# Optimization experiments

Hardware: AMD Instinct MI355X
Metric: run time of the kernel (lower is better)

The kernel has to match this reference:

```python
import jax, jax.numpy as jnp
import numpy as np

S, I, C_M, C_P, C_Z = 128, 384, 256, 32, 128

def setup_inputs() -> dict:
    key = jax.random.key(0)
    ks = jax.random.split(key, 7)
    sc = 1.0 / np.sqrt(C_M)
    return {
        "msa_rep": jax.random.normal(ks[0], (S, I, C_M), jnp.float32),
        "ln_gamma": jnp.ones((C_M,), jnp.float32),
        "ln_beta": jnp.zeros((C_M,), jnp.float32),
        "Wa": jax.random.normal(ks[1], (C_P, C_M), jnp.float32) * sc,
        "Wb": jax.random.normal(ks[2], (C_P, C_M), jnp.float32) * sc,
        "Wproj": jax.random.normal(ks[3], (C_Z, C_P * C_P), jnp.float32) / np.sqrt(C_P * C_P),
        "bproj": jnp.zeros((C_Z,), jnp.float32),
    }

def reference(msa_rep, ln_gamma, ln_beta, Wa, Wb, Wproj, bproj):
    # LayerNorm over last dim (eps matches torch default 1e-5)
    mu = jnp.mean(msa_rep, axis=-1, keepdims=True)
    var = jnp.mean(jnp.square(msa_rep - mu), axis=-1, keepdims=True)
    x = (msa_rep - mu) * jax.lax.rsqrt(var + 1e-5) * ln_gamma + ln_beta
    # Two linear projections (torch Linear: y = x @ W.T), no bias
    a = jnp.einsum('sic,pc->sip', x, Wa)  # [s, i, c_p]
    b = jnp.einsum('sic,pc->sip', x, Wb)  # [s, i, c_p]
    norm = 1.0 / msa_rep.shape[-3]
    # Outer product mean over sequences s -> [i, j, c, d]
    outer = norm * jnp.einsum('sic,sjd->ijcd', a, b)
    outer = outer.reshape(outer.shape[0], outer.shape[1], -1)  # [i, j, c*c]
    return jnp.einsum('ijk,zk->ijz', outer, Wproj) + bproj  # [i, j, c_z]
```

## Files before the change

### kernel.cpp

```cpp
#include <hip/hip_runtime.h>
#include <hip/hip_bf16.h>

typedef short s8v  __attribute__((ext_vector_type(8)));
typedef float f32x4 __attribute__((ext_vector_type(4)));

__device__ __forceinline__ unsigned short f2bf(float f) {
  unsigned int b = __float_as_uint(f);
  b += 0x7fffu + ((b >> 16) & 1u);
  return (unsigned short)(b >> 16);
}

__global__ __launch_bounds__(256) void prep_w_kernel(
    const float* __restrict__ Wa, const float* __restrict__ Wb,
    const float* __restrict__ Wproj,
    unsigned short* __restrict__ wab, unsigned short* __restrict__ wfrag) {
  int gid = blockIdx.x * 256 + threadIdx.x;
  if (gid < 16384) {
    int e = gid;
    int j = e & 7, lane = (e >> 3) & 63, kt = (e >> 9) & 7, nt = e >> 12;
    int p = nt * 16 + (lane & 15);
    int c = kt * 32 + ((lane >> 4) << 3) + j;
    float v = (p < 32) ? Wa[p * 256 + c] : Wb[(p - 32) * 256 + c];
    wab[e] = f2bf(v);
  } else {
    int e = gid - 16384;
    int j = e & 7, lane = (e >> 3) & 63, kt = (e >> 9) & 31, nt = e >> 14;
    int z = nt * 16 + (lane & 15);
    int kp = kt * 32 + ((lane >> 4) << 3) + j;
    int c = kp & 31, d = kp >> 5;
    wfrag[e] = f2bf(Wproj[z * 1024 + c * 32 + d]);
  }
}

#define XS 264
#define OS 66
__global__ __launch_bounds__(256) void kernel_a(
    const float* __restrict__ msa, const float* __restrict__ gamma, const float* __restrict__ beta,
    const unsigned short* __restrict__ wab,
    unsigned short* __restrict__ afrag, unsigned short* __restrict__ bfrag) {
  __shared__ unsigned short xs[64 * XS];
  __shared__ float os[64 * OS];
  const int i  = blockIdx.x >> 1;
  const int sh = blockIdx.x & 1;
  const int tid = threadIdx.x;
  const int w = tid >> 6, lane = tid & 63;
  const int gq = lane >> 4, nlo = lane & 15;

  const float4 g4  = *(const float4*)(gamma + lane * 4);
  const float4 be4 = *(const float4*)(beta  + lane * 4);

  for (int it = 0; it < 16; ++it) {
    const int sl = it * 4 + w;
    const int s  = sh * 64 + sl;
    const float4 v = *(const float4*)(msa + (size_t)(s * 384 + i) * 256 + lane * 4);
    float sum = v.x + v.y + v.z + v.w;
    float sq  = fmaf(v.x, v.x, fmaf(v.y, v.y, fmaf(v.z, v.z, v.w * v.w)));
#pragma unroll
    for (int off = 32; off >= 1; off >>= 1) {
      sum += __shfl_xor(sum, off);
      sq  += __shfl_xor(sq,  off);
    }
    const float mu   = sum * (1.f / 256.f);
    const float var  = sq * (1.f / 256.f) - mu * mu;
    const float rstd = rsqrtf(var + 1e-5f);
    unsigned int lo = (unsigned int)f2bf((v.x - mu) * rstd * g4.x + be4.x)
                    | ((unsigned int)f2bf((v.y - mu) * rstd * g4.y + be4.y) << 16);
    unsigned int hi = (unsigned int)f2bf((v.z - mu) * rstd * g4.z + be4.z)
                    | ((unsigned int)f2bf((v.w - mu) * rstd * g4.w + be4.w) << 16);
    *(uint2*)&xs[sl * XS + lane * 4] = make_uint2(lo, hi);
  }
  __syncthreads();

  const f32x4 z4 = {0.f, 0.f, 0.f, 0.f};
  f32x4 acc[4];
#pragma unroll
  for (int nt = 0; nt < 4; ++nt) acc[nt] = z4;
  for (int kt = 0; kt < 8; ++kt) {
    const s8v av = *(const s8v*)&xs[(w * 16 + nlo) * XS + kt * 32 + gq * 8];
#pragma unroll
    for (int nt = 0; nt < 4; ++nt) {
      const s8v bv = ((const s8v*)wab)[(nt * 8 + kt) * 64 + lane];
      acc[nt] = __builtin_amdgcn_mfma_f32_16x16x32_bf16(av, bv, acc[nt], 0, 0, 0);
    }
  }
#pragma unroll
  for (int nt = 0; nt < 4; ++nt)
#pragma unroll
    for (int r = 0; r < 4; ++r)
      os[(w * 16 + gq * 4 + r) * OS + nt * 16 + nlo] = acc[nt][r];
  __syncthreads();

#pragma unroll
  for (int q = 0; q < 2; ++q) {
    const int set = q * 256 + tid;
    const int lf  = set & 63;
    const int ktl = (set >> 6) & 1;
    const int hi2 = (set >> 7) & 1;
    const int mat = (set >> 8) & 1;
    const int g2  = lf >> 4;
    const int p   = mat * 32 + (lf & 15) + 16 * hi2;
    s8v pk;
#pragma unroll
    for (int j = 0; j < 8; ++j) {
      const int srow = ktl * 32 + g2 * 8 + j;
      pk[j] = (short)f2bf(os[srow * OS + p]);
    }
    unsigned short* dst = mat ? bfrag : afrag;
    const int rb = i * 2 + hi2;
    const int kt = sh * 2 + ktl;
    *(s8v*)(dst + ((size_t)((rb * 4 + kt) * 64 + lf)) * 8) = pk;
  }
}

#define TS5 520
__global__ __launch_bounds__(512, 4) void kernel_main(
    const unsigned short* __restrict__ afrag, const unsigned short* __restrict__ bfrag,
    const unsigned short* __restrict__ wfrag, const float* __restrict__ bproj,
    float* __restrict__ out) {
  extern __shared__ unsigned short t[];
  const int bid = (blockIdx.x & 7) * 288 + (blockIdx.x >> 3);
  const int bi = bid / 48, bj = bid % 48;
  const int tid = threadIdx.x;
  const int wave = tid >> 6, lane = tid & 63;
  const int wm = wave >> 1, wn = wave & 1;
  const int gq = lane >> 4, nlo = lane & 15;

  const s8v* ag = (const s8v*)afrag;
  const s8v* bg = (const s8v*)bfrag;
  const s8v* wg = (const s8v*)wfrag;
  const f32x4 z4 = {0.f, 0.f, 0.f, 0.f};

  f32x4 acc2[4];
#pragma unroll
  for (int mt = 0; mt < 4; ++mt) acc2[mt] = z4;

#pragma unroll 1
  for (int dc = 0; dc < 2; ++dc) {
#pragma unroll 1
    for (int ph = 0; ph < 2; ++ph) {
      f32x4 acc[4][2];
#pragma unroll
      for (int mt = 0; mt < 4; ++mt) { acc[mt][0] = z4; acc[mt][1] = z4; }
#pragma unroll 2
      for (int kt = 0; kt < 4; ++kt) {
        s8v av[4];
#pragma unroll
        for (int mt = 0; mt < 4; ++mt)
          av[mt] = ag[((bi * 16 + wm * 4 + mt) * 4 + kt) * 64 + lane];
        s8v bv[2];
#pragma unroll
        for (int nt = 0; nt < 2; ++nt)
          bv[nt] = bg[(((bj * 8 + ph * 4 + wn * 2 + nt) * 2 + dc) * 4 + kt) * 64 + lane];
#pragma unroll
        for (int mt = 0; mt < 4; ++mt)
#pragma unroll
          for (int nt = 0; nt < 2; ++nt)
            acc[mt][nt] = __builtin_amdgcn_mfma_f32_16x16x32_bf16(av[mt], bv[nt], acc[mt][nt], 0, 0, 0);
      }
      if (dc && ph == 0) __syncthreads();
#pragma unroll
      for (int mt = 0; mt < 4; ++mt) {
        const int row0 = (wm * 2 + (mt >> 1)) * 8 + ph * 4 + wn * 2;
        const int c0 = (mt & 1) * 16 + 4 * gq;
        const int hw = nlo * 32 + (c0 ^ (8 * ((nlo >> 1) & 3)));
#pragma unroll
        for (int nt = 0; nt < 2; ++nt) {
          const unsigned int lo = (unsigned int)f2bf(acc[mt][nt][0] * 0.0078125f)
                                | ((unsigned int)f2bf(acc[mt][nt][1] * 0.0078125f) << 16);
          const unsigned int hi = (unsigned int)f2bf(acc[mt][nt][2] * 0.0078125f)
                                | ((unsigned int)f2bf(acc[mt][nt][3] * 0.0078125f) << 16);
          *(uint2*)&t[(row0 + nt) * TS5 + hw] = make_uint2(lo, hi);
        }
      }
    }
    __syncthreads();

#pragma unroll 2
    for (int kt2 = 0; kt2 < 16; ++kt2) {
      const int hwb = kt2 * 32 + 8 * (gq ^ ((kt2 >> 1) & 3));
      const s8v wv = wg[(wave * 32 + dc * 16 + kt2) * 64 + lane];
      s8v av2[4];
#pragma unroll
      for (int mt = 0; mt < 4; ++mt)
        av2[mt] = *(const s8v*)&t[(mt * 16 + nlo) * TS5 + hwb];
#pragma unroll
      for (int mt = 0; mt < 4; ++mt)
        acc2[mt] = __builtin_amdgcn_mfma_f32_16x16x32_bf16(av2[mt], wv, acc2[mt], 0, 0, 0);
    }
    if (!dc) __syncthreads();
  }

  const int z = wave * 16 + nlo;
  const float bz = bproj[z];
#pragma unroll
  for (int mt = 0; mt < 4; ++mt)
#pragma unroll
    for (int r = 0; r < 4; ++r) {
      const int ij = mt * 16 + gq * 4 + r;
      const int gi = bi * 8 + (ij >> 3), gj = bj * 8 + (ij & 7);
      out[(size_t)(gi * 384 + gj) * 128 + z] = acc2[mt][r] + bz;
    }
}

extern "C" void kernel_launch(void* const* d_in, const int* in_sizes, int n_in,
                              void* d_out, int out_size, void* d_ws, size_t ws_size,
                              hipStream_t stream) {
  const float* msa   = (const float*)d_in[0];
  const float* gam   = (const float*)d_in[1];
  const float* bet   = (const float*)d_in[2];
  const float* Wa    = (const float*)d_in[3];
  const float* Wb    = (const float*)d_in[4];
  const float* Wproj = (const float*)d_in[5];
  const float* bpr   = (const float*)d_in[6];
  float* out = (float*)d_out;

  if (ws_size < 6586368) return;
  unsigned short* afrag = (unsigned short*)d_ws;
  unsigned short* bfrag = afrag + 1572864;
  unsigned short* wab   = bfrag + 1572864;
  unsigned short* wfr   = wab + 16384;

  (void)hipFuncSetAttribute(reinterpret_cast<const void*>(kernel_main),
                            hipFuncAttributeMaxDynamicSharedMemorySize, 64 * TS5 * 2);

  prep_w_kernel<<<576, 256, 0, stream>>>(Wa, Wb, Wproj, wab, wfr);
  kernel_a<<<768, 256, 0, stream>>>(msa, gam, bet, wab, afrag, bfrag);
  kernel_main<<<2304, 512, 64 * TS5 * 2, stream>>>(afrag, bfrag, wfr, bpr, out);
}
```

Measured before the change: 149.2 us.

## Switch main kernel to 32x32x16 MFMA with 1024-thread blocks and split-K reduction

Re-layouts the a/b and Wproj fragments for the 32x32x16 bf16 MFMA. The main kernel now builds the full 64x1024 outer-product tile in LDS in one pass instead of two d-chunk passes. The projection step is split over K across 16 waves, and the partial sums are reduced through LDS. This is meant to cut instruction count and redundant fragment loads, at the cost of a larger LDS footprint, an extra reduction and sync stage, and 1024-thread blocks that may lower occupancy. It also drops the block-index swizzle used for L2 locality.

```diff
diff --git a/kernel.cpp b/kernel.cpp
--- a/kernel.cpp
+++ b/kernel.cpp
@@ -1,8 +1,9 @@
 #include <hip/hip_runtime.h>
 #include <hip/hip_bf16.h>
 
-typedef short s8v  __attribute__((ext_vector_type(8)));
+typedef short s8v   __attribute__((ext_vector_type(8)));
 typedef float f32x4 __attribute__((ext_vector_type(4)));
+typedef float f32x16 __attribute__((ext_vector_type(16)));
 
 __device__ __forceinline__ unsigned short f2bf(float f) {
   unsigned int b = __float_as_uint(f);
@@ -24,10 +25,10 @@
     wab[e] = f2bf(v);
   } else {
     int e = gid - 16384;
-    int j = e & 7, lane = (e >> 3) & 63, kt = (e >> 9) & 31, nt = e >> 14;
-    int z = nt * 16 + (lane & 15);
-    int kp = kt * 32 + ((lane >> 4) << 3) + j;
-    int c = kp & 31, d = kp >> 5;
+    int j = e & 7, lane = (e >> 3) & 63, kt2 = (e >> 9) & 63, zt = e >> 15;
+    int z = zt * 32 + (lane & 31);
+    int kpp = kt2 * 16 + ((lane >> 5) << 3) + j;
+    int d = kpp >> 5, c = kpp & 31;
     wfrag[e] = f2bf(Wproj[z * 1024 + c * 32 + d]);
   }
 }
@@ -94,112 +95,121 @@
   for (int q = 0; q < 2; ++q) {
     const int set = q * 256 + tid;
     const int lf  = set & 63;
-    const int ktl = (set >> 6) & 1;
-    const int hi2 = (set >> 7) & 1;
-    const int mat = (set >> 8) & 1;
-    const int g2  = lf >> 4;
-    const int p   = mat * 32 + (lf & 15) + 16 * hi2;
+    const int ktl = (set >> 6) & 3;
+    const int mat = set >> 8;
+    const int gg  = lf >> 5;
+    const int p   = mat * 32 + (lf & 31);
     s8v pk;
 #pragma unroll
-    for (int j = 0; j < 8; ++j) {
-      const int srow = ktl * 32 + g2 * 8 + j;
-      pk[j] = (short)f2bf(os[srow * OS + p]);
-    }
+    for (int j = 0; j < 8; ++j)
+      pk[j] = (short)f2bf(os[(ktl * 16 + 8 * gg + j) * OS + p]);
     unsigned short* dst = mat ? bfrag : afrag;
-    const int rb = i * 2 + hi2;
-    const int kt = sh * 2 + ktl;
-    *(s8v*)(dst + ((size_t)((rb * 4 + kt) * 64 + lf)) * 8) = pk;
-  }
-}
-
-#define TS5 520
-__global__ __launch_bounds__(512, 4) void kernel_main(
+    *(s8v*)(dst + ((size_t)((i * 8 + sh * 4 + ktl) * 64 + lf)) * 8) = pk;
+  }
+}
+
+#define TSM 1032
+__global__ __launch_bounds__(1024, 4) void kernel_main(
     const unsigned short* __restrict__ afrag, const unsigned short* __restrict__ bfrag,
     const unsigned short* __restrict__ wfrag, const float* __restrict__ bproj,
     float* __restrict__ out) {
   extern __shared__ unsigned short t[];
-  const int bid = (blockIdx.x & 7) * 288 + (blockIdx.x >> 3);
+  const int bid = blockIdx.x;
   const int bi = bid / 48, bj = bid % 48;
   const int tid = threadIdx.x;
   const int wave = tid >> 6, lane = tid & 63;
-  const int wm = wave >> 1, wn = wave & 1;
-  const int gq = lane >> 4, nlo = lane & 15;
+  const int g = lane >> 5, l31 = lane & 31;
 
   const s8v* ag = (const s8v*)afrag;
   const s8v* bg = (const s8v*)bfrag;
   const s8v* wg = (const s8v*)wfrag;
-  const f32x4 z4 = {0.f, 0.f, 0.f, 0.f};
-
-  f32x4 acc2[4];
-#pragma unroll
-  for (int mt = 0; mt < 4; ++mt) acc2[mt] = z4;
-
-#pragma unroll 1
-  for (int dc = 0; dc < 2; ++dc) {
-#pragma unroll 1
-    for (int ph = 0; ph < 2; ++ph) {
-      f32x4 acc[4][2];
-#pragma unroll
-      for (int mt = 0; mt < 4; ++mt) { acc[mt][0] = z4; acc[mt][1] = z4; }
+
+  {
+    const int wm = wave >> 2, wn = wave & 3;
+    f32x16 a00 = {}, a01 = {}, a10 = {}, a11 = {};
 #pragma unroll 2
-      for (int kt = 0; kt < 4; ++kt) {
-        s8v av[4];
-#pragma unroll
-        for (int mt = 0; mt < 4; ++mt)
-          av[mt] = ag[((bi * 16 + wm * 4 + mt) * 4 + kt) * 64 + lane];
-        s8v bv[2];
-#pragma unroll
-        for (int nt = 0; nt < 2; ++nt)
-          bv[nt] = bg[(((bj * 8 + ph * 4 + wn * 2 + nt) * 2 + dc) * 4 + kt) * 64 + lane];
-#pragma unroll
-        for (int mt = 0; mt < 4; ++mt)
-#pragma unroll
-          for (int nt = 0; nt < 2; ++nt)
-            acc[mt][nt] = __builtin_amdgcn_mfma_f32_16x16x32_bf16(av[mt], bv[nt], acc[mt][nt], 0, 0, 0);
-      }
-      if (dc && ph == 0) __syncthreads();
-#pragma unroll
-      for (int mt = 0; mt < 4; ++mt) {
-        const int row0 = (wm * 2 + (mt >> 1)) * 8 + ph * 4 + wn * 2;
-        const int c0 = (mt & 1) * 16 + 4 * gq;
-        const int hw = nlo * 32 + (c0 ^ (8 * ((nlo >> 1) & 3)));
-#pragma unroll
-        for (int nt = 0; nt < 2; ++nt) {
-          const unsigned int lo = (unsigned int)f2bf(acc[mt][nt][0] * 0.0078125f)
-                                | ((unsigned int)f2bf(acc[mt][nt][1] * 0.0078125f) << 16);
-          const unsigned int hi = (unsigned int)f2bf(acc[mt][nt][2] * 0.0078125f)
-                                | ((unsigned int)f2bf(acc[mt][nt][3] * 0.0078125f) << 16);
-          *(uint2*)&t[(row0 + nt) * TS5 + hw] = make_uint2(lo, hi);
+    for (int kt = 0; kt < 8; ++kt) {
+      const s8v av0 = ag[((bi * 8 + wm * 2 + 0) * 8 + kt) * 64 + lane];
+      const s8v av1 = ag[((bi * 8 + wm * 2 + 1) * 8 + kt) * 64 + lane];
+      const s8v bv0 = bg[((bj * 8 + wn * 2 + 0) * 8 + kt) * 64 + lane];
+      const s8v bv1 = bg[((bj * 8 + wn * 2 + 1) * 8 + kt) * 64 + lane];
+      a00 = __builtin_amdgcn_mfma_f32_32x32x16_bf16(av0, bv0, a00, 0, 0, 0);
+      a01 = __builtin_amdgcn_mfma_f32_32x32x16_bf16(av0, bv1, a01, 0, 0, 0);
+      a10 = __builtin_amdgcn_mfma_f32_32x32x16_bf16(av1, bv0, a10, 0, 0, 0);
+      a11 = __builtin_amdgcn_mfma_f32_32x32x16_bf16(av1, bv1, a11, 0, 0, 0);
+    }
+    const int xr = 8 * (l31 & 3);
+#pragma unroll
+    for (int mt = 0; mt < 2; ++mt)
+#pragma unroll
+      for (int nt = 0; nt < 2; ++nt) {
+        const f32x16& a = (mt == 0) ? (nt == 0 ? a00 : a01) : (nt == 0 ? a10 : a11);
+        const int row_t = (wm * 2 + mt) * 8 + wn * 2 + nt;
+#pragma unroll
+        for (int q = 0; q < 4; ++q) {
+          const int c0 = q * 8 + 4 * g;
+          const int hw = l31 * 32 + (c0 ^ xr);
+          const unsigned int lo = (unsigned int)f2bf(a[q * 4 + 0] * 0.0078125f)
+                                | ((unsigned int)f2bf(a[q * 4 + 1] * 0.0078125f) << 16);
+          const unsigned int hi = (unsigned int)f2bf(a[q * 4 + 2] * 0.0078125f)
+                                | ((unsigned int)f2bf(a[q * 4 + 3] * 0.0078125f) << 16);
+          *(uint2*)&t[row_t * TSM + hw] = make_uint2(lo, hi);
         }
       }
-    }
-    __syncthreads();
-
-#pragma unroll 2
-    for (int kt2 = 0; kt2 < 16; ++kt2) {
-      const int hwb = kt2 * 32 + 8 * (gq ^ ((kt2 >> 1) & 3));
-      const s8v wv = wg[(wave * 32 + dc * 16 + kt2) * 64 + lane];
-      s8v av2[4];
-#pragma unroll
-      for (int mt = 0; mt < 4; ++mt)
-        av2[mt] = *(const s8v*)&t[(mt * 16 + nlo) * TS5 + hwb];
-#pragma unroll
-      for (int mt = 0; mt < 4; ++mt)
-        acc2[mt] = __builtin_amdgcn_mfma_f32_16x16x32_bf16(av2[mt], wv, acc2[mt], 0, 0, 0);
-    }
-    if (!dc) __syncthreads();
-  }
-
-  const int z = wave * 16 + nlo;
-  const float bz = bproj[z];
-#pragma unroll
-  for (int mt = 0; mt < 4; ++mt)
-#pragma unroll
-    for (int r = 0; r < 4; ++r) {
-      const int ij = mt * 16 + gq * 4 + r;
-      const int gi = bi * 8 + (ij >> 3), gj = bj * 8 + (ij & 7);
-      out[(size_t)(gi * 384 + gj) * 128 + z] = acc2[mt][r] + bz;
-    }
+  }
+  __syncthreads();
+
+  const int zt = wave & 3, kh = wave >> 2;
+  f32x16 p0 = {}, p1 = {};
+#pragma unroll 4
+  for (int k2 = 0; k2 < 16; ++k2) {
+    const int kt2 = kh * 16 + k2;
+    const int d = kt2 >> 1;
+    const int hwb = d * 32 + ((((kt2 & 1) * 16) + 8 * g) ^ (8 * (d & 3)));
+    const s8v wv = wg[((zt * 64 + kt2) * 64 + lane)];
+    const s8v a0 = *(const s8v*)&t[l31 * TSM + hwb];
+    const s8v a1 = *(const s8v*)&t[(32 + l31) * TSM + hwb];
+    p0 = __builtin_amdgcn_mfma_f32_32x32x16_bf16(a0, wv, p0, 0, 0, 0);
+    p1 = __builtin_amdgcn_mfma_f32_32x32x16_bf16(a1, wv, p1, 0, 0, 0);
+  }
+  __syncthreads();
+
+  float* sc = (float*)t;
+  if (kh > 0) {
+    const int slot = zt * 3 + (kh - 1);
+#pragma unroll
+    for (int r = 0; r < 16; ++r) {
+      sc[((slot * 2 + 0) * 16 + r) * 64 + lane] = p0[r];
+      sc[((slot * 2 + 1) * 16 + r) * 64 + lane] = p1[r];
+    }
+  }
+  __syncthreads();
+  if (kh == 0) {
+#pragma unroll
+    for (int s2 = 0; s2 < 3; ++s2) {
+      const int slot = zt * 3 + s2;
+#pragma unroll
+      for (int r = 0; r < 16; ++r) {
+        p0[r] += sc[((slot * 2 + 0) * 16 + r) * 64 + lane];
+        p1[r] += sc[((slot * 2 + 1) * 16 + r) * 64 + lane];
+      }
+    }
+    const int z = zt * 32 + l31;
+    const float bz = bproj[z];
+#pragma unroll
+    for (int r = 0; r < 16; ++r) {
+      {
+        const int ij = (r & 3) + 8 * (r >> 2) + 4 * g;
+        const int gi = bi * 8 + (ij >> 3), gj = bj * 8 + (ij & 7);
+        out[(size_t)(gi * 384 + gj) * 128 + z] = p0[r] + bz;
+      }
+      {
+        const int ij = 32 + (r & 3) + 8 * (r >> 2) + 4 * g;
+        const int gi = bi * 8 + (ij >> 3), gj = bj * 8 + (ij & 7);
+        out[(size_t)(gi * 384 + gj) * 128 + z] = p1[r] + bz;
+      }
+    }
+  }
 }
 
 extern "C" void kernel_launch(void* const* d_in, const int* in_sizes, int n_in,
@@ -221,9 +231,9 @@
   unsigned short* wfr   = wab + 16384;
 
   (void)hipFuncSetAttribute(reinterpret_cast<const void*>(kernel_main),
-                            hipFuncAttributeMaxDynamicSharedMemorySize, 64 * TS5 * 2);
+                            hipFuncAttributeMaxDynamicSharedMemorySize, 64 * TSM * 2);
 
   prep_w_kernel<<<576, 256, 0, stream>>>(Wa, Wb, Wproj, wab, wfr);
   kernel_a<<<768, 256, 0, stream>>>(msa, gam, bet, wab, afrag, bfrag);
-  kernel_main<<<2304, 512, 64 * TS5 * 2, stream>>>(afrag, bfrag, wfr, bpr, out);
-}
+  kernel_main<<<2304, 1024, 64 * TSM * 2, stream>>>(afrag, bfrag, wfr, bpr, out);
+}
```

Result: faster. 134.8 us (median of 2 runs) (-9.7%).
